# Performance work log

Hardware: AMD Instinct MI355X
Metric: run time of the kernel (lower is better)

Reference implementation:

```python
import jax, jax.numpy as jnp
import numpy as np
from jax import lax

B, T, H, C = 1024, 1024, 256, 10

def setup_inputs() -> dict:
    key = jax.random.key(0)
    k = jax.random.split(key, 6)
    return {
        "x": jax.random.normal(k[0], (B, T), dtype=jnp.float32),
        "W_hx": jax.random.normal(k[1], (H, 1), dtype=jnp.float32),
        "W_hh": jax.random.normal(k[2], (H, H), dtype=jnp.float32),
        "b_h": jax.random.normal(k[3], (H,), dtype=jnp.float32),
        "W_hp": jax.random.normal(k[4], (C, H), dtype=jnp.float32),
        "b_o": jax.random.normal(k[5], (C,), dtype=jnp.float32),
    }

def reference(x, W_hx, W_hh, b_h, W_hp, b_o):
    # x: [B, T] (input_dim hard-coded to 1 in the original: x[:, t].unsqueeze(1))
    # torch.einsum('bh,hh->bh', h, W_hh) == h * diag(W_hh)  (repeated 'hh' index)
    w_diag = jnp.einsum('hh->h', W_hh)          # [H] loop-invariant, hoisted
    w_in = W_hx[:, 0]                            # [H]
    h0 = jnp.zeros((x.shape[0], w_in.shape[0]), dtype=x.dtype)

    def step(h, x_t):
        # einsum('bn,hn->bh', x_t[:,None], W_hx) with n=1 is an outer product
        h_new = jnp.tanh(x_t[:, None] * w_in + h * w_diag + b_h)
        return h_new, None

    h_final, _ = lax.scan(step, h0, x.T)         # scan over time: xs [T, B]
    return jnp.einsum('bh,ch->bc', h_final, W_hp) + b_o  # [B, C]
```

## Files before the change

kernel.cpp:

```cpp
#include <hip/hip_runtime.h>
#include <math.h>

#define BB 1024
#define TT 1024
#define HH 256
#define CC 10


__global__ __launch_bounds__(HH) void vanilla_rnn_kernel(
    const float* __restrict__ x,
    const float* __restrict__ W_hx,
    const float* __restrict__ W_hh,
    const float* __restrict__ b_h,
    const float* __restrict__ W_hp,
    const float* __restrict__ b_o,
    float* __restrict__ out)
{
    __shared__ float xs0[TT + 8];
    __shared__ float xs1[TT + 8];
    __shared__ float part[2][CC * 4];

    const int tid = threadIdx.x;
    const int b0  = blockIdx.x * 2;

    ((float4*)xs0)[tid] = ((const float4*)(x + (size_t)b0 * TT))[tid];
    ((float4*)xs1)[tid] = ((const float4*)(x + (size_t)(b0 + 1) * TT))[tid];
    if (tid < 2) {
        ((float4*)xs0)[TT / 4 + tid] = make_float4(0.f, 0.f, 0.f, 0.f);
        ((float4*)xs1)[TT / 4 + tid] = make_float4(0.f, 0.f, 0.f, 0.f);
    }

    const float S    = 2.88539008177792681472f;
    const float winS = W_hx[tid] * S;
    const float wd   = W_hh[tid * HH + tid];
    const float A    = -2.0f * wd * S;
    const float bhS2 = (b_h[tid] + wd) * S;
    float whp[CC];
#pragma unroll
    for (int c = 0; c < CC; ++c) whp[c] = W_hp[c * HH + tid];

    __syncthreads();

    float r0 = 0.5f, r1 = 0.5f;
    const float4* xa = (const float4*)xs0;
    const float4* xb = (const float4*)xs1;
    float4 curA = xa[0], nxtA = xa[1];
    float4 curB = xb[0], nxtB = xb[1];
#pragma unroll 4
    for (int t4 = 0; t4 < TT / 4; ++t4) {
        float4 pfA = xa[t4 + 2];
        float4 pfB = xb[t4 + 2];
        float qa0 = fmaf(curA.x, winS, bhS2);
        float qa1 = fmaf(curA.y, winS, bhS2);
        float qa2 = fmaf(curA.z, winS, bhS2);
        float qa3 = fmaf(curA.w, winS, bhS2);
        float qb0 = fmaf(curB.x, winS, bhS2);
        float qb1 = fmaf(curB.y, winS, bhS2);
        float qb2 = fmaf(curB.z, winS, bhS2);
        float qb3 = fmaf(curB.w, winS, bhS2);
        float m0, m1, t0, t1;
        m0 = fmaf(A, r0, qa0);                  m1 = fmaf(A, r1, qb0);
        t0 = __builtin_amdgcn_exp2f(m0);        t1 = __builtin_amdgcn_exp2f(m1);
        r0 = __builtin_amdgcn_rcpf(t0 + 1.0f);  r1 = __builtin_amdgcn_rcpf(t1 + 1.0f);
        m0 = fmaf(A, r0, qa1);                  m1 = fmaf(A, r1, qb1);
        t0 = __builtin_amdgcn_exp2f(m0);        t1 = __builtin_amdgcn_exp2f(m1);
        r0 = __builtin_amdgcn_rcpf(t0 + 1.0f);  r1 = __builtin_amdgcn_rcpf(t1 + 1.0f);
        m0 = fmaf(A, r0, qa2);                  m1 = fmaf(A, r1, qb2);
        t0 = __builtin_amdgcn_exp2f(m0);        t1 = __builtin_amdgcn_exp2f(m1);
        r0 = __builtin_amdgcn_rcpf(t0 + 1.0f);  r1 = __builtin_amdgcn_rcpf(t1 + 1.0f);
        m0 = fmaf(A, r0, qa3);                  m1 = fmaf(A, r1, qb3);
        t0 = __builtin_amdgcn_exp2f(m0);        t1 = __builtin_amdgcn_exp2f(m1);
        r0 = __builtin_amdgcn_rcpf(t0 + 1.0f);  r1 = __builtin_amdgcn_rcpf(t1 + 1.0f);
        curA = nxtA; nxtA = pfA;
        curB = nxtB; nxtB = pfB;
    }
    float h0 = fmaf(-2.0f, r0, 1.0f);
    float h1 = fmaf(-2.0f, r1, 1.0f);

    const int lane = tid & 63;
    const int wave = tid >> 6;
#pragma unroll
    for (int c = 0; c < CC; ++c) {
        float v0 = h0 * whp[c];
        float v1 = h1 * whp[c];
#pragma unroll
        for (int off = 32; off >= 1; off >>= 1) {
            v0 += __shfl_down(v0, off);
            v1 += __shfl_down(v1, off);
        }
        if (lane == 0) { part[0][c * 4 + wave] = v0; part[1][c * 4 + wave] = v1; }
    }
    __syncthreads();

    if (tid < 2 * CC) {
        const int bb = tid / CC;
        const int c  = tid - bb * CC;
        float acc = b_o[c];
#pragma unroll
        for (int w = 0; w < 4; ++w) acc += part[bb][c * 4 + w];
        out[(size_t)(b0 + bb) * CC + c] = acc;
    }
}

extern "C" void kernel_launch(void* const* d_in, const int* in_sizes, int n_in,
                              void* d_out, int out_size, void* d_ws, size_t ws_size,
                              hipStream_t stream) {
    const float* x    = (const float*)d_in[0];
    const float* W_hx = (const float*)d_in[1];
    const float* W_hh = (const float*)d_in[2];
    const float* b_h  = (const float*)d_in[3];
    const float* W_hp = (const float*)d_in[4];
    const float* b_o  = (const float*)d_in[5];
    float* out = (float*)d_out;

    vanilla_rnn_kernel<<<BB / 2, HH, 0, stream>>>(x, W_hx, W_hh, b_h, W_hp, b_o, out);
}
```

Measured before the change: 117.9 us.

## Stream x from global memory with prefetch and pack two chains into packed-FP32 ops

Removes the LDS staging of both input rows and the block barrier, and instead reads x directly from global memory as float4 with a two-ahead register prefetch. The prefetch index is clamped so it never reads past the row. The two independent batch recurrences are packed into 2-wide float vectors so the FMA and add can map to packed FP32 instructions. The loop unroll factor drops from 4 to 2. This trades LDS traffic and the barrier for global loads on the serial recurrence path, which risks exposing memory latency if the prefetch distance is too short.

```diff
diff --git a/kernel.cpp b/kernel.cpp
--- a/kernel.cpp
+++ b/kernel.cpp
@@ -6,6 +6,8 @@
 #define HH 256
 #define CC 10
 
+
+typedef float f2 __attribute__((ext_vector_type(2)));
 
 __global__ __launch_bounds__(HH) void vanilla_rnn_kernel(
     const float* __restrict__ x,
@@ -16,19 +18,10 @@
     const float* __restrict__ b_o,
     float* __restrict__ out)
 {
-    __shared__ float xs0[TT + 8];
-    __shared__ float xs1[TT + 8];
     __shared__ float part[2][CC * 4];
 
     const int tid = threadIdx.x;
     const int b0  = blockIdx.x * 2;
-
-    ((float4*)xs0)[tid] = ((const float4*)(x + (size_t)b0 * TT))[tid];
-    ((float4*)xs1)[tid] = ((const float4*)(x + (size_t)(b0 + 1) * TT))[tid];
-    if (tid < 2) {
-        ((float4*)xs0)[TT / 4 + tid] = make_float4(0.f, 0.f, 0.f, 0.f);
-        ((float4*)xs1)[TT / 4 + tid] = make_float4(0.f, 0.f, 0.f, 0.f);
-    }
 
     const float S    = 2.88539008177792681472f;
     const float winS = W_hx[tid] * S;
@@ -39,43 +32,45 @@
 #pragma unroll
     for (int c = 0; c < CC; ++c) whp[c] = W_hp[c * HH + tid];
 
-    __syncthreads();
+    const float4* __restrict__ xA = (const float4*)(x + (size_t)b0 * TT);
+    const float4* __restrict__ xB = (const float4*)(x + (size_t)(b0 + 1) * TT);
 
-    float r0 = 0.5f, r1 = 0.5f;
-    const float4* xa = (const float4*)xs0;
-    const float4* xb = (const float4*)xs1;
-    float4 curA = xa[0], nxtA = xa[1];
-    float4 curB = xb[0], nxtB = xb[1];
-#pragma unroll 4
-    for (int t4 = 0; t4 < TT / 4; ++t4) {
-        float4 pfA = xa[t4 + 2];
-        float4 pfB = xb[t4 + 2];
-        float qa0 = fmaf(curA.x, winS, bhS2);
-        float qa1 = fmaf(curA.y, winS, bhS2);
-        float qa2 = fmaf(curA.z, winS, bhS2);
-        float qa3 = fmaf(curA.w, winS, bhS2);
-        float qb0 = fmaf(curB.x, winS, bhS2);
-        float qb1 = fmaf(curB.y, winS, bhS2);
-        float qb2 = fmaf(curB.z, winS, bhS2);
-        float qb3 = fmaf(curB.w, winS, bhS2);
-        float m0, m1, t0, t1;
-        m0 = fmaf(A, r0, qa0);                  m1 = fmaf(A, r1, qb0);
-        t0 = __builtin_amdgcn_exp2f(m0);        t1 = __builtin_amdgcn_exp2f(m1);
-        r0 = __builtin_amdgcn_rcpf(t0 + 1.0f);  r1 = __builtin_amdgcn_rcpf(t1 + 1.0f);
-        m0 = fmaf(A, r0, qa1);                  m1 = fmaf(A, r1, qb1);
-        t0 = __builtin_amdgcn_exp2f(m0);        t1 = __builtin_amdgcn_exp2f(m1);
-        r0 = __builtin_amdgcn_rcpf(t0 + 1.0f);  r1 = __builtin_amdgcn_rcpf(t1 + 1.0f);
-        m0 = fmaf(A, r0, qa2);                  m1 = fmaf(A, r1, qb2);
-        t0 = __builtin_amdgcn_exp2f(m0);        t1 = __builtin_amdgcn_exp2f(m1);
-        r0 = __builtin_amdgcn_rcpf(t0 + 1.0f);  r1 = __builtin_amdgcn_rcpf(t1 + 1.0f);
-        m0 = fmaf(A, r0, qa3);                  m1 = fmaf(A, r1, qb3);
-        t0 = __builtin_amdgcn_exp2f(m0);        t1 = __builtin_amdgcn_exp2f(m1);
-        r0 = __builtin_amdgcn_rcpf(t0 + 1.0f);  r1 = __builtin_amdgcn_rcpf(t1 + 1.0f);
-        curA = nxtA; nxtA = pfA;
-        curB = nxtB; nxtB = pfB;
+    f2 r  = (f2){0.5f, 0.5f};
+    const f2 A2   = (f2){A, A};
+    const f2 one2 = (f2){1.0f, 1.0f};
+
+    float4 curA = xA[0], curB = xB[0];
+    float4 nxtA = xA[1], nxtB = xB[1];
+
+#pragma unroll 2
+    for (int i = 0; i < TT / 4; ++i) {
+        int ip = i + 2;
+        if (ip > TT / 4 - 1) ip = TT / 4 - 1;
+        float4 pfA = xA[ip];
+        float4 pfB = xB[ip];
+
+        f2 q, m, t, u;
+#define STEP(XA, XB)                                   \
+        q.x = fmaf((XA), winS, bhS2);                  \
+        q.y = fmaf((XB), winS, bhS2);                  \
+        m   = __builtin_elementwise_fma(A2, r, q);     \
+        t.x = __builtin_amdgcn_exp2f(m.x);             \
+        t.y = __builtin_amdgcn_exp2f(m.y);             \
+        u   = t + one2;                                \
+        r.x = __builtin_amdgcn_rcpf(u.x);              \
+        r.y = __builtin_amdgcn_rcpf(u.y);
+
+        STEP(curA.x, curB.x)
+        STEP(curA.y, curB.y)
+        STEP(curA.z, curB.z)
+        STEP(curA.w, curB.w)
+#undef STEP
+
+        curA = nxtA; curB = nxtB;
+        nxtA = pfA;  nxtB = pfB;
     }
-    float h0 = fmaf(-2.0f, r0, 1.0f);
-    float h1 = fmaf(-2.0f, r1, 1.0f);
+    float h0 = fmaf(-2.0f, r.x, 1.0f);
+    float h1 = fmaf(-2.0f, r.y, 1.0f);
 
     const int lane = tid & 63;
     const int wave = tid >> 6;
```

New measurement: 129.0 us. 9.5% more time.
